# Performance work log

Measured on AMD Instinct MI355X. Metric: run time of the kernel, lower is better.

Reference implementation:

```python
import jax, jax.numpy as jnp
import numpy as np
import math

B, T, E, H = 4, 4096, 1024, 16
D = E // H  # head dim
EPS_DENOM = 1e-6
LN_EPS = 1e-5


def setup_inputs() -> dict:
    key = jax.random.key(0)
    ks = jax.random.split(key, 8)
    s = 0.02
    return {
        "x": jax.random.normal(ks[0], (B, T, E), jnp.float32),
        "ln1_w": jnp.ones((E,), jnp.float32),
        "ln1_b": jnp.zeros((E,), jnp.float32),
        "wq": jax.random.normal(ks[1], (E, E), jnp.float32) * s,
        "bq": jnp.zeros((E,), jnp.float32),
        "wk": jax.random.normal(ks[2], (E, E), jnp.float32) * s,
        "bk": jnp.zeros((E,), jnp.float32),
        "wv": jax.random.normal(ks[3], (E, E), jnp.float32) * s,
        "bv": jnp.zeros((E,), jnp.float32),
        "wo": jax.random.normal(ks[4], (E, E), jnp.float32) * s,
        "bo": jnp.zeros((E,), jnp.float32),
        "ln2_w": jnp.ones((E,), jnp.float32),
        "ln2_b": jnp.zeros((E,), jnp.float32),
        "w_fc": jax.random.normal(ks[5], (E, 4 * E), jnp.float32) * s,
        "b_fc": jnp.zeros((4 * E,), jnp.float32),
        "w_proj": jax.random.normal(ks[6], (4 * E, E), jnp.float32) * s,
        "b_proj": jnp.zeros((E,), jnp.float32),
    }


def _layernorm(x, w, b):
    mu = jnp.mean(x, axis=-1, keepdims=True)
    var = jnp.mean(jnp.square(x - mu), axis=-1, keepdims=True)
    return (x - mu) * jax.lax.rsqrt(var + LN_EPS) * w + b


def _cosformer_attn(x, wq, bq, wk, bk, wv, bv, wo, bo):
    # ReLU feature map on q, k projections
    q = jax.nn.relu(x @ wq + bq)  # [B,T,E]
    k = jax.nn.relu(x @ wk + bk)
    v = x @ wv + bv
    # split heads -> [B,H,T,D]
    q = q.reshape(B, T, H, D).transpose(0, 2, 1, 3)
    k = k.reshape(B, T, H, D).transpose(0, 2, 1, 3)
    v = v.reshape(B, T, H, D).transpose(0, 2, 1, 3)
    # cosine reweighting: idx_i = pi/2 * (i+1)/M, M = T (self-attention)
    idx = (math.pi / 2.0) * jnp.arange(1, T + 1, dtype=x.dtype) / T  # [T]
    s = jnp.sin(idx)[None, None, :, None]
    c = jnp.cos(idx)[None, None, :, None]
    q_ = jnp.concatenate([q * s, q * c], axis=-1)  # [B,H,T,2D]
    k_ = jnp.concatenate([k * s, k * c], axis=-1)  # [B,H,T,2D]
    # non-causal linear attention: O = Q' (K'^T V) / (Q' K'^T 1)
    kv = jnp.einsum("bhtd,bhte->bhde", k_, v)       # [B,H,2D,D]
    z = 1.0 / jnp.maximum(jnp.einsum("bhtd,bhd->bht", q_, k_.sum(axis=2)), EPS_DENOM)
    out = jnp.einsum("bhtd,bhde,bht->bhte", q_, kv, z)  # [B,H,T,D]
    out = out.transpose(0, 2, 1, 3).reshape(B, T, E)
    return out @ wo + bo


def reference(x, ln1_w, ln1_b, wq, bq, wk, bk, wv, bv, wo, bo,
              ln2_w, ln2_b, w_fc, b_fc, w_proj, b_proj):
    h = _layernorm(x, ln1_w, ln1_b)
    x = x + _cosformer_attn(h, wq, bq, wk, bk, wv, bv, wo, bo)
    h = _layernorm(x, ln2_w, ln2_b)
    h = jax.nn.gelu(h @ w_fc + b_fc, approximate=False) @ w_proj + b_proj
    return x + h
```

## Files before the change

kernel.cpp:

```cpp
#include <hip/hip_runtime.h>

#define PI_F 3.14159265358979f
#define MT 16384
#define EE 1024
#define FF 4096
#define NCH 8
#define CHT (4096 / NCH)

typedef unsigned short u16;
typedef __attribute__((ext_vector_type(8))) short short8;
typedef __attribute__((ext_vector_type(4))) float f32x4;

__device__ __forceinline__ float bf2f(u16 u) {
  unsigned int v = ((unsigned int)u) << 16;
  float f;
  __builtin_memcpy(&f, &v, 4);
  return f;
}
__device__ __forceinline__ u16 f2bf(float f) {
  unsigned int x;
  __builtin_memcpy(&x, &f, 4);
  unsigned int r = x + 0x7fffu + ((x >> 16) & 1u);
  return (u16)(r >> 16);
}
__device__ __forceinline__ float ldin(const void* p, long i, int f32) {
  return f32 ? ((const float*)p)[i] : bf2f(((const u16*)p)[i]);
}
__device__ __forceinline__ void async16(const u16* g, u16* l) {
  __builtin_amdgcn_global_load_lds(
      (const __attribute__((address_space(1))) unsigned int*)g,
      (__attribute__((address_space(3))) unsigned int*)l, 16, 0, 0);
}

__global__ __launch_bounds__(256) void detect_dtype(const u16* __restrict__ x,
                                                    int* __restrict__ flag) {
  const int tid = threadIdx.x;
  int cnt = 0;
  for (int i = tid; i < 2048; i += 256) {
    const int e = (x[i] >> 7) & 0xFF;
    if (e == 0 || e >= 0x90) cnt++;
  }
#pragma unroll
  for (int o = 32; o > 0; o >>= 1) cnt += __shfl_xor(cnt, o);
  __shared__ int s[4];
  if ((tid & 63) == 0) s[tid >> 6] = cnt;
  __syncthreads();
  if (tid == 0) flag[0] = (s[0] + s[1] + s[2] + s[3] > 200) ? 1 : 0;
}

__global__ __launch_bounds__(256) void transpose_in(
    const void* __restrict__ src, const int* __restrict__ flag,
    u16* __restrict__ dst, int R, int C) {
  __shared__ float tile[64][65];
  const int f = *flag;
  const int tx = threadIdx.x & 63, ty = threadIdx.x >> 6;
  const long c0 = (long)blockIdx.x * 64, r0 = (long)blockIdx.y * 64;
#pragma unroll
  for (int i = 0; i < 16; i++) {
    const int r = ty + i * 4;
    tile[r][tx] = ldin(src, (r0 + r) * (long)C + c0 + tx, f);
  }
  __syncthreads();
#pragma unroll
  for (int i = 0; i < 16; i++) {
    const int cc = ty + i * 4;
    dst[(c0 + cc) * (long)R + r0 + tx] = f2bf(tile[tx][cc]);
  }
}

__global__ __launch_bounds__(256) void concat3(
    const void* __restrict__ a, const void* __restrict__ b,
    const void* __restrict__ c, const int* __restrict__ flag,
    float* __restrict__ out) {
  const int i = blockIdx.x * 256 + threadIdx.x;
  const int fl = *flag;
  if (i < 1024) out[i] = ldin(a, i, fl);
  else if (i < 2048) out[i] = ldin(b, i - 1024, fl);
  else if (i < 3072) out[i] = ldin(c, i - 2048, fl);
}

__global__ __launch_bounds__(256) void ln_kernel(
    const void* __restrict__ xin, int xmode, const int* __restrict__ flag,
    const void* __restrict__ w, const void* __restrict__ b,
    u16* __restrict__ out) {
  const long row = blockIdx.x;
  const int tid = threadIdx.x;
  const int fl = *flag;
  const int xf = (xmode == 2) ? fl : xmode;
  float v[4];
  if (xf) {
    const float4 q = ((const float4*)((const float*)xin + row * EE))[tid];
    v[0] = q.x; v[1] = q.y; v[2] = q.z; v[3] = q.w;
  } else {
    const ushort4 u = ((const ushort4*)((const u16*)xin + row * EE))[tid];
    v[0] = bf2f(u.x); v[1] = bf2f(u.y); v[2] = bf2f(u.z); v[3] = bf2f(u.w);
  }
  float sum = v[0] + v[1] + v[2] + v[3];
  float sq = v[0] * v[0] + v[1] * v[1] + v[2] * v[2] + v[3] * v[3];
#pragma unroll
  for (int o = 32; o > 0; o >>= 1) {
    sum += __shfl_xor(sum, o);
    sq += __shfl_xor(sq, o);
  }
  __shared__ float s1[4], s2[4];
  const int wave = tid >> 6, lane = tid & 63;
  if (lane == 0) { s1[wave] = sum; s2[wave] = sq; }
  __syncthreads();
  sum = s1[0] + s1[1] + s1[2] + s1[3];
  sq = s2[0] + s2[1] + s2[2] + s2[3];
  const float mu = sum * (1.f / EE);
  const float var = sq * (1.f / EE) - mu * mu;
  const float rs = rsqrtf(var + 1e-5f);
  ushort4 o4;
  float r0 = (v[0] - mu) * rs * ldin(w, tid * 4 + 0, fl) + ldin(b, tid * 4 + 0, fl);
  float r1 = (v[1] - mu) * rs * ldin(w, tid * 4 + 1, fl) + ldin(b, tid * 4 + 1, fl);
  float r2 = (v[2] - mu) * rs * ldin(w, tid * 4 + 2, fl) + ldin(b, tid * 4 + 2, fl);
  float r3 = (v[3] - mu) * rs * ldin(w, tid * 4 + 3, fl) + ldin(b, tid * 4 + 3, fl);
  o4.x = f2bf(r0); o4.y = f2bf(r1); o4.z = f2bf(r2); o4.w = f2bf(r3);
  ((ushort4*)(out + row * EE))[tid] = o4;
}

__global__ __launch_bounds__(512, 2) void gemm256(
    const u16* __restrict__ A, const u16* __restrict__ Bt,
    const void* __restrict__ bias, int biasF32,
    const void* __restrict__ res, int resMode,
    void* __restrict__ Cout, void* __restrict__ Cv, int outMode, long coff,
    const int* __restrict__ flag, int M, int N, int K, int act) {
  __shared__ u16 As[3][2][4096];
  __shared__ u16 Bs[3][2][4096];
  const int tid = threadIdx.x;
  const int lane = tid & 63;
  const int wave = tid >> 6;
  const int wr = wave >> 2;
  const int wc = wave & 3;
  const int quad = lane >> 4;
  const int l16 = lane & 15;
  const int bid0 = blockIdx.x + gridDim.x * blockIdx.y;
  const int width = 4 * gridDim.y;
  const int group = bid0 / width;
  const int rem = bid0 - group * width;
  const int bx = group * 4 + (rem & 3);
  const int by = rem >> 2;
  const long bm = (long)bx * 256;
  const long bn = (long)by * 256;

  f32x4 acc[8][4];
#pragma unroll
  for (int i = 0; i < 8; i++)
#pragma unroll
    for (int j = 0; j < 4; j++)
#pragma unroll
      for (int r = 0; r < 4; r++) acc[i][j][r] = 0.f;

  const int sr = tid >> 2;
  const int su = tid & 3;
  const u16* Ap = A + (bm + sr) * (long)K + su * 8;
  const u16* Bp = Bt + (bn + sr) * (long)K + su * 8;
  const long half128 = 128 * (long)K;

  auto stgA = [&](int d, int h, long kt) {
    async16(Ap + h * half128 + kt, &As[d][h][0] + wave * 512);
  };
  auto stgB = [&](int d, int h, long kt) {
    async16(Bp + h * half128 + kt, &Bs[d][h][0] + wave * 512);
  };

  const int nt = K >> 5;
  stgA(0, 0, 0); stgA(0, 1, 0); stgB(0, 0, 0); stgB(0, 1, 0);
  stgA(1, 0, 32); stgA(1, 1, 32); stgB(1, 0, 32); stgB(1, 1, 32);
  asm volatile("s_waitcnt vmcnt(4)" ::: "memory");
  __builtin_amdgcn_s_barrier();

  int d = 0;
  for (int t = 0; t < nt; ++t) {
    const int sd = (t + 2) % 3;
    const long skt = ((t + 2 < nt) ? (long)(t + 2) : (long)(nt - 1)) * 32;
    const u16* Ah = &As[d][wr][0];
    short8 af[4], bfr[4];
#pragma unroll
    for (int i = 0; i < 4; i++)
      af[i] = *(const short8*)&Ah[(i * 16 + l16) * 32 + quad * 8];
#pragma unroll
    for (int ni = 0; ni < 4; ni++) {
      const int cl = wc * 64 + ni * 16 + l16;
      bfr[ni] = *(const short8*)&Bs[d][cl >> 7][(cl & 127) * 32 + quad * 8];
    }
    stgA(sd, 0, skt);
    stgA(sd, 1, skt);
    asm volatile("s_waitcnt vmcnt(4)" ::: "memory");
    __builtin_amdgcn_s_barrier();
    __builtin_amdgcn_s_setprio(1);
#pragma unroll
    for (int mi = 0; mi < 4; mi++)
#pragma unroll
      for (int ni = 0; ni < 4; ni++)
        acc[mi][ni] = __builtin_amdgcn_mfma_f32_16x16x32_bf16(
            af[mi], bfr[ni], acc[mi][ni], 0, 0, 0);
    __builtin_amdgcn_s_setprio(0);
    __builtin_amdgcn_s_barrier();
#pragma unroll
    for (int i = 0; i < 4; i++)
      af[i] = *(const short8*)&Ah[(64 + i * 16 + l16) * 32 + quad * 8];
    stgB(sd, 0, skt);
    stgB(sd, 1, skt);
    asm volatile("s_waitcnt vmcnt(4)" ::: "memory");
    __builtin_amdgcn_s_barrier();
    __builtin_amdgcn_s_setprio(1);
#pragma unroll
    for (int mi = 0; mi < 4; mi++)
#pragma unroll
      for (int ni = 0; ni < 4; ni++)
        acc[4 + mi][ni] = __builtin_amdgcn_mfma_f32_16x16x32_bf16(
            af[mi], bfr[ni], acc[4 + mi][ni], 0, 0, 0);
    __builtin_amdgcn_s_setprio(0);
    __builtin_amdgcn_s_barrier();
    d = (d == 2) ? 0 : d + 1;
  }
  __syncthreads();

  const int fl = *flag;
  const long Nl = N;
  float bv4[4];
  long gcA[4];
#pragma unroll
  for (int ni = 0; ni < 4; ni++) {
    gcA[ni] = bn + wc * 64 + ni * 16 + l16;
    bv4[ni] = biasF32 ? ((const float*)bias)[gcA[ni]] : ldin(bias, gcA[ni], fl);
  }
#pragma unroll
  for (int mi = 0; mi < 8; mi++)
#pragma unroll
    for (int ni = 0; ni < 4; ni++)
#pragma unroll
      for (int r = 0; r < 4; r++) {
        float v = acc[mi][ni][r] + bv4[ni];
        if (act == 1 || (act == 3 && gcA[ni] < 2048)) v = fmaxf(v, 0.f);
        else if (act == 2) v = 0.5f * v * (1.f + erff(v * 0.70710678118654752f));
        acc[mi][ni][r] = v;
      }
  float* sf = (float*)&As[0][0][0] + wave * 1088;
  const int er = lane >> 2;
  const int ec = (lane & 3) * 16;
#pragma unroll
  for (int mi = 0; mi < 8; mi++) {
#pragma unroll
    for (int ni = 0; ni < 4; ni++)
#pragma unroll
      for (int r = 0; r < 4; r++)
        sf[(quad * 4 + r) * 68 + ni * 16 + l16] = acc[mi][ni][r];
    f32x4 w0 = *(const f32x4*)&sf[er * 68 + ec + 0];
    f32x4 w1 = *(const f32x4*)&sf[er * 68 + ec + 4];
    f32x4 w2 = *(const f32x4*)&sf[er * 68 + ec + 8];
    f32x4 w3 = *(const f32x4*)&sf[er * 68 + ec + 12];
    const long gr = bm + wr * 128 + mi * 16 + er;
    const long gc0 = bn + wc * 64 + ec;
    const long ib = gr * Nl + gc0;
    if (resMode == 1 || (resMode == 2 && fl)) {
      const f32x4* rp = (const f32x4*)((const float*)res + ib);
      f32x4 r0 = rp[0], r1 = rp[1], r2 = rp[2], r3 = rp[3];
#pragma unroll
      for (int j = 0; j < 4; j++) {
        w0[j] += r0[j]; w1[j] += r1[j]; w2[j] += r2[j]; w3[j] += r3[j];
      }
    } else if (resMode == 2) {
      const short8* rp = (const short8*)((const u16*)res + ib);
      short8 ra = rp[0], rb = rp[1];
#pragma unroll
      for (int j = 0; j < 4; j++) {
        w0[j] += bf2f((u16)ra[j]);
        w1[j] += bf2f((u16)ra[j + 4]);
        w2[j] += bf2f((u16)rb[j]);
        w3[j] += bf2f((u16)rb[j + 4]);
      }
    }
    if (outMode == 1 || (outMode == 2 && fl)) {
      f32x4* op = (f32x4*)((float*)Cout + coff + ib);
      op[0] = w0; op[1] = w1; op[2] = w2; op[3] = w3;
    } else {
      u16 tmp[16];
#pragma unroll
      for (int j = 0; j < 4; j++) {
        tmp[j] = f2bf(w0[j]);
        tmp[j + 4] = f2bf(w1[j]);
        tmp[j + 8] = f2bf(w2[j]);
        tmp[j + 12] = f2bf(w3[j]);
      }
      u16* op;
      if (outMode == 3) {
        const int plane = (int)(gc0 >> 10);
        u16* dst = (plane == 2) ? (u16*)Cv
                                : ((u16*)Cout + plane * ((long)M << 10));
        op = dst + (gr << 10) + (gc0 & 1023);
      } else {
        op = (u16*)Cout + coff + ib;
      }
      *(short8*)op = *(short8*)&tmp[0];
      *(short8*)(op + 8) = *(short8*)&tmp[8];
    }
  }
}

__global__ __launch_bounds__(256, 3) void gemm_bf16(
    const u16* __restrict__ A, const u16* __restrict__ Bt,
    const void* __restrict__ bias, int biasF32,
    const void* __restrict__ res, int resMode,
    void* __restrict__ Cout, void* __restrict__ Cv, int outMode, long coff,
    const int* __restrict__ flag, int M, int N, int K, int act) {
  __shared__ u16 As[3][4096];
  __shared__ u16 Bs[3][4096];
  const int tid = threadIdx.x;
  const int lane = tid & 63;
  const int wave = tid >> 6;
  const int quad = lane >> 4;
  const int l16 = lane & 15;
  const int wm = (wave >> 1) * 64;
  const int wn = (wave & 1) * 64;
  const int bid0 = blockIdx.x + gridDim.x * blockIdx.y;
  const int gy = gridDim.y;
  const int width = 8 * gy;
  const int group = bid0 / width;
  const int rem = bid0 - group * width;
  const int bx = group * 8 + (rem & 7);
  const int by = rem >> 3;
  const long bm = (long)bx * 128;
  const long bn = (long)by * 128;

  f32x4 acc[4][4];
#pragma unroll
  for (int i = 0; i < 4; i++)
#pragma unroll
    for (int j = 0; j < 4; j++)
#pragma unroll
      for (int r = 0; r < 4; r++) acc[i][j][r] = 0.f;

  const int trow = tid >> 2;
  const int tswz = (tid & 3) ^ (trow & 3);
  const u16* Ap = A + (bm + trow) * (long)K + tswz * 8;
  const u16* Bp = Bt + (bn + trow) * (long)K + tswz * 8;
  const long rowK64 = 64 * (long)K;

  auto stage = [&](int buf, long kt) {
    u16* Ad = &As[buf][wave * 512];
    u16* Bd = &Bs[buf][wave * 512];
    async16(Ap + kt, Ad);
    async16(Ap + rowK64 + kt, Ad + 2048);
    async16(Bp + kt, Bd);
    async16(Bp + rowK64 + kt, Bd + 2048);
  };
  const int rswz = (quad ^ (l16 & 3)) * 8;
  auto compute = [&](int buf) {
    short8 af[4], bfr[4];
#pragma unroll
    for (int i = 0; i < 4; i++)
      af[i] = *(const short8*)&As[buf][(wm + i * 16 + l16) * 32 + rswz];
#pragma unroll
    for (int i = 0; i < 4; i++)
      bfr[i] = *(const short8*)&Bs[buf][(wn + i * 16 + l16) * 32 + rswz];
    __builtin_amdgcn_s_setprio(1);
#pragma unroll
    for (int mi = 0; mi < 4; mi++)
#pragma unroll
      for (int ni = 0; ni < 4; ni++)
        acc[mi][ni] = __builtin_amdgcn_mfma_f32_16x16x32_bf16(
            af[mi], bfr[ni], acc[mi][ni], 0, 0, 0);
    __builtin_amdgcn_s_setprio(0);
  };

  const int nt = K >> 5;
  stage(0, 0);
  stage(1, 32);
  asm volatile("s_waitcnt vmcnt(4)" ::: "memory");
  __builtin_amdgcn_s_barrier();
  int cb = 0, sb = 2;
  for (int t = 0; t < nt; ++t) {
    const long ts = (t + 2 < nt) ? (long)(t + 2) * 32 : (long)(nt - 1) * 32;
    stage(sb, ts);
    compute(cb);
    asm volatile("s_waitcnt vmcnt(4)" ::: "memory");
    __builtin_amdgcn_s_barrier();
    cb = (cb == 2) ? 0 : cb + 1;
    sb = (sb == 2) ? 0 : sb + 1;
  }
  __syncthreads();

  const int fl = *flag;
  const long Nl = N;
  float bv4[4];
  long gcA[4];
#pragma unroll
  for (int ni = 0; ni < 4; ni++) {
    gcA[ni] = bn + wn + ni * 16 + l16;
    bv4[ni] = biasF32 ? ((const float*)bias)[gcA[ni]] : ldin(bias, gcA[ni], fl);
  }
#pragma unroll
  for (int mi = 0; mi < 4; mi++)
#pragma unroll
    for (int ni = 0; ni < 4; ni++)
#pragma unroll
      for (int r = 0; r < 4; r++) {
        float v = acc[mi][ni][r] + bv4[ni];
        if (act == 1 || (act == 3 && gcA[ni] < 2048)) v = fmaxf(v, 0.f);
        else if (act == 2) v = 0.5f * v * (1.f + erff(v * 0.70710678118654752f));
        acc[mi][ni][r] = v;
      }
  float* sf = (float*)&As[0][0] + wave * 1088;
  const int er = lane >> 2;
  const int ec = (lane & 3) * 16;
#pragma unroll
  for (int mi = 0; mi < 4; mi++) {
#pragma unroll
    for (int ni = 0; ni < 4; ni++)
#pragma unroll
      for (int r = 0; r < 4; r++)
        sf[(quad * 4 + r) * 68 + ni * 16 + l16] = acc[mi][ni][r];
    f32x4 w0 = *(const f32x4*)&sf[er * 68 + ec + 0];
    f32x4 w1 = *(const f32x4*)&sf[er * 68 + ec + 4];
    f32x4 w2 = *(const f32x4*)&sf[er * 68 + ec + 8];
    f32x4 w3 = *(const f32x4*)&sf[er * 68 + ec + 12];
    const long gr = bm + wm + mi * 16 + er;
    const long gc0 = bn + wn + ec;
    const long ib = gr * Nl + gc0;
    if (resMode == 1 || (resMode == 2 && fl)) {
      const f32x4* rp = (const f32x4*)((const float*)res + ib);
      f32x4 r0 = rp[0], r1 = rp[1], r2 = rp[2], r3 = rp[3];
#pragma unroll
      for (int j = 0; j < 4; j++) {
        w0[j] += r0[j]; w1[j] += r1[j]; w2[j] += r2[j]; w3[j] += r3[j];
      }
    } else if (resMode == 2) {
      const short8* rp = (const short8*)((const u16*)res + ib);
      short8 ra = rp[0], rb = rp[1];
#pragma unroll
      for (int j = 0; j < 4; j++) {
        w0[j] += bf2f((u16)ra[j]);
        w1[j] += bf2f((u16)ra[j + 4]);
        w2[j] += bf2f((u16)rb[j]);
        w3[j] += bf2f((u16)rb[j + 4]);
      }
    }
    if (outMode == 1 || (outMode == 2 && fl)) {
      f32x4* op = (f32x4*)((float*)Cout + coff + ib);
      op[0] = w0; op[1] = w1; op[2] = w2; op[3] = w3;
    } else {
      u16 tmp[16];
#pragma unroll
      for (int j = 0; j < 4; j++) {
        tmp[j] = f2bf(w0[j]);
        tmp[j + 4] = f2bf(w1[j]);
        tmp[j + 8] = f2bf(w2[j]);
        tmp[j + 12] = f2bf(w3[j]);
      }
      u16* op;
      if (outMode == 3) {
        const int plane = (int)(bn >> 10);
        u16* dst = (plane == 2) ? (u16*)Cv
                                : ((u16*)Cout + plane * ((long)M << 10));
        op = dst + (gr << 10) + (gc0 & 1023);
      } else {
        op = (u16*)Cout + coff + ib;
      }
      *(short8*)op = *(short8*)&tmp[0];
      *(short8*)(op + 8) = *(short8*)&tmp[8];
    }
  }
}

__global__ __launch_bounds__(256) void kv_partial(
    const u16* __restrict__ k, const u16* __restrict__ v,
    float* __restrict__ kvpart, float* __restrict__ kspart) {
  const int bh = blockIdx.x;
  const int ch = blockIdx.y;
  const int b = bh >> 4, h = bh & 15;
  const int tid = threadIdx.x;
  __shared__ float kl[8][64], vl[8][64];
  const int dkq = tid >> 4;
  const int dvq = tid & 15;
  float accS[4][4] = {}, accC[4][4] = {};
  float ksS[4] = {}, ksC[4] = {};
  const int tt = tid >> 5;
  const int cc = (tid & 31) * 2;
  const long base = ((long)b * 4096 + ch * CHT) * EE + h * 64;
  for (int tb = 0; tb < CHT; tb += 8) {
    const long roff = base + (long)(tb + tt) * EE + cc;
    const unsigned int ku = *(const unsigned int*)(k + roff);
    const unsigned int vu = *(const unsigned int*)(v + roff);
    __syncthreads();
    kl[tt][cc] = bf2f((u16)ku);
    kl[tt][cc + 1] = bf2f((u16)(ku >> 16));
    vl[tt][cc] = bf2f((u16)vu);
    vl[tt][cc + 1] = bf2f((u16)(vu >> 16));
    __syncthreads();
#pragma unroll
    for (int j = 0; j < 8; j++) {
      const int t = ch * CHT + tb + j;
      float s, c;
      __sincosf((float)(t + 1) * (PI_F * 0.5f / 4096.f), &s, &c);
      float kk[4], vv[4];
#pragma unroll
      for (int i = 0; i < 4; i++) {
        kk[i] = kl[j][dkq * 4 + i];
        vv[i] = vl[j][dvq * 4 + i];
      }
#pragma unroll
      for (int i = 0; i < 4; i++) {
        const float ks_ = kk[i] * s, kc_ = kk[i] * c;
        ksS[i] += ks_;
        ksC[i] += kc_;
#pragma unroll
        for (int jj = 0; jj < 4; jj++) {
          accS[i][jj] += ks_ * vv[jj];
          accC[i][jj] += kc_ * vv[jj];
        }
      }
    }
  }
  float* outS = kvpart + (((long)ch * 64 + bh) * 2 + 0) * 4096;
  float* outC = outS + 4096;
#pragma unroll
  for (int i = 0; i < 4; i++)
#pragma unroll
    for (int jj = 0; jj < 4; jj++) {
      outS[(dkq * 4 + i) * 64 + dvq * 4 + jj] = accS[i][jj];
      outC[(dkq * 4 + i) * 64 + dvq * 4 + jj] = accC[i][jj];
    }
  if (dvq == 0) {
    float* oS = kspart + ((long)ch * 64 + bh) * 2 * 64;
#pragma unroll
    for (int i = 0; i < 4; i++) {
      oS[dkq * 4 + i] = ksS[i];
      oS[64 + dkq * 4 + i] = ksC[i];
    }
  }
}

__global__ __launch_bounds__(256) void kv_reduce(
    const float* __restrict__ kvpart, const float* __restrict__ kspart,
    float* __restrict__ kvcomb, float* __restrict__ kscomb) {
  const long KVTOT = 64L * 2 * 4096;
  const long KSTOT = 64L * 2 * 64;
  const long idx = (long)blockIdx.x * 256 + threadIdx.x;
  if (idx < KVTOT) {
    float s = 0.f;
#pragma unroll
    for (int chn = 0; chn < NCH; chn++) s += kvpart[chn * KVTOT + idx];
    kvcomb[idx] = s;
  } else {
    const long i2 = idx - KVTOT;
    if (i2 < KSTOT) {
      float s = 0.f;
#pragma unroll
      for (int chn = 0; chn < NCH; chn++) s += kspart[chn * KSTOT + i2];
      kscomb[i2] = s;
    }
  }
}

__global__ __launch_bounds__(256) void attn_apply(
    const u16* __restrict__ q, const float* __restrict__ kvcomb,
    const float* __restrict__ kscomb, u16* __restrict__ attn) {
  const int bh = blockIdx.x;
  const int b = bh >> 4, h = bh & 15;
  const int t0 = blockIdx.y * 64;
  const int tid = threadIdx.x;
  __shared__ float kvl[2][64][64];
  __shared__ float ksl[2][64];
  __shared__ float ql[64][66];

  const float4* kvsrc = (const float4*)(kvcomb + (long)bh * 8192);
  float4* kvdst = (float4*)&kvl[0][0][0];
#pragma unroll
  for (int i = 0; i < 8; i++) kvdst[tid + 256 * i] = kvsrc[tid + 256 * i];
  if (tid < 32) ((float4*)&ksl[0][0])[tid] = ((const float4*)(kscomb + (long)bh * 128))[tid];
  {
    const int r = tid >> 2;
    const int c = (tid & 3) * 16;
    const u16* qp = q + ((long)b * 4096 + t0 + r) * EE + h * 64 + c;
    const uint4 u0 = *(const uint4*)qp;
    const uint4 u1 = *(const uint4*)(qp + 8);
    unsigned int uu[8] = {u0.x, u0.y, u0.z, u0.w, u1.x, u1.y, u1.z, u1.w};
#pragma unroll
    for (int i = 0; i < 8; i++) {
      ql[r][c + 2 * i] = bf2f((u16)uu[i]);
      ql[r][c + 2 * i + 1] = bf2f((u16)(uu[i] >> 16));
    }
  }
  __syncthreads();

  const int tg = tid >> 4;
  const int dvq = tid & 15;
  const int dv0 = dvq * 4;

  float o1[4][4] = {}, o2[4][4] = {}, zs[4] = {}, zc[4] = {};
  for (int dk = 0; dk < 64; dk++) {
    const float ks0 = ksl[0][dk], ks1 = ksl[1][dk];
    float kv0[4], kv1[4];
#pragma unroll
    for (int j = 0; j < 4; j++) {
      kv0[j] = kvl[0][dk][dv0 + j];
      kv1[j] = kvl[1][dk][dv0 + j];
    }
#pragma unroll
    for (int it = 0; it < 4; it++) {
      const float qv = ql[tg + it * 16][dk];
      zs[it] += qv * ks0;
      zc[it] += qv * ks1;
#pragma unroll
      for (int j = 0; j < 4; j++) {
        o1[it][j] += qv * kv0[j];
        o2[it][j] += qv * kv1[j];
      }
    }
  }
#pragma unroll
  for (int it = 0; it < 4; it++) {
    const int t = t0 + tg + it * 16;
    float s, c;
    __sincosf((float)(t + 1) * (PI_F * 0.5f / 4096.f), &s, &c);
    const float z = s * zs[it] + c * zc[it];
    const float zinv = 1.f / fmaxf(z, 1e-6f);
    ushort4 o4;
    o4.x = f2bf((s * o1[it][0] + c * o2[it][0]) * zinv);
    o4.y = f2bf((s * o1[it][1] + c * o2[it][1]) * zinv);
    o4.z = f2bf((s * o1[it][2] + c * o2[it][2]) * zinv);
    o4.w = f2bf((s * o1[it][3] + c * o2[it][3]) * zinv);
    *(ushort4*)(attn + ((long)b * 4096 + t) * EE + h * 64 + dv0) = o4;
  }
}

extern "C" void kernel_launch(void* const* d_in, const int* in_sizes, int n_in,
                              void* d_out, int out_size, void* d_ws, size_t ws_size,
                              hipStream_t stream) {
  const void* x = d_in[0];
  const void* ln1w = d_in[1];
  const void* ln1b = d_in[2];
  const void* wq = d_in[3];
  const void* bq = d_in[4];
  const void* wk = d_in[5];
  const void* bk = d_in[6];
  const void* wv = d_in[7];
  const void* bv = d_in[8];
  const void* wo = d_in[9];
  const void* bo = d_in[10];
  const void* ln2w = d_in[11];
  const void* ln2b = d_in[12];
  const void* wfc = d_in[13];
  const void* bfc = d_in[14];
  const void* wproj = d_in[15];
  const void* bproj = d_in[16];

  char* ws = (char*)d_ws;
  size_t off = 0;
  auto alloc = [&](size_t bytes) -> char* {
    char* p = ws + off;
    off += (bytes + 255) & ~((size_t)255);
    return p;
  };
  int* flag = (int*)alloc(256);
  u16* wqkvT = (u16*)alloc((size_t)3 * EE * EE * 2);
  u16* woT = (u16*)alloc((size_t)EE * EE * 2);
  u16* wfcT = (u16*)alloc((size_t)EE * FF * 2);
  u16* wprojT = (u16*)alloc((size_t)FF * EE * 2);
  float* qkvBias = (float*)alloc(3072 * 4);
  u16* h = (u16*)alloc((size_t)MT * EE * 2);
  float* x2 = (float*)alloc((size_t)MT * EE * 4);
  u16* qk2 = (u16*)alloc((size_t)2 * MT * EE * 2);
  float* kvpart = (float*)alloc((size_t)NCH * 64 * 2 * 64 * 64 * 4);
  float* kspart = (float*)alloc((size_t)NCH * 64 * 2 * 64 * 4);
  float* kvcomb = (float*)alloc((size_t)64 * 2 * 64 * 64 * 4);
  float* kscomb = (float*)alloc((size_t)64 * 2 * 64 * 4);
  const long PL = (long)MT * EE;
  u16* qb = qk2;
  u16* kb = qk2 + PL;
  u16* vb = (u16*)x2;
  u16* attnb = kb;
  u16* g = qk2;
  (void)ws_size; (void)in_sizes; (void)n_in; (void)out_size;

  detect_dtype<<<1, 256, 0, stream>>>((const u16*)x, flag);

  transpose_in<<<dim3(16, 16), 256, 0, stream>>>(wq, flag, wqkvT, EE, EE);
  transpose_in<<<dim3(16, 16), 256, 0, stream>>>(wk, flag, wqkvT + (size_t)EE * EE, EE, EE);
  transpose_in<<<dim3(16, 16), 256, 0, stream>>>(wv, flag, wqkvT + (size_t)2 * EE * EE, EE, EE);
  transpose_in<<<dim3(16, 16), 256, 0, stream>>>(wo, flag, woT, EE, EE);
  transpose_in<<<dim3(64, 16), 256, 0, stream>>>(wfc, flag, wfcT, EE, FF);
  transpose_in<<<dim3(16, 64), 256, 0, stream>>>(wproj, flag, wprojT, FF, EE);
  concat3<<<12, 256, 0, stream>>>(bq, bk, bv, flag, qkvBias);

  ln_kernel<<<MT, 256, 0, stream>>>(x, 2, flag, ln1w, ln1b, h);

  gemm256<<<dim3(64, 12), 512, 0, stream>>>(h, wqkvT, qkvBias, 1, nullptr, 0,
                                            qk2, vb, 3, 0, flag, MT, 3072, EE, 3);

  kv_partial<<<dim3(64, NCH), 256, 0, stream>>>(kb, vb, kvpart, kspart);
  kv_reduce<<<2080, 256, 0, stream>>>(kvpart, kspart, kvcomb, kscomb);
  attn_apply<<<dim3(64, 64), 256, 0, stream>>>(qb, kvcomb, kscomb, attnb);

  gemm256<<<dim3(64, 4), 512, 0, stream>>>(attnb, woT, bo, 0, x, 2, x2, nullptr,
                                           1, 0, flag, MT, EE, EE, 0);
  ln_kernel<<<MT, 256, 0, stream>>>(x2, 1, flag, ln2w, ln2b, h);

  for (int c = 0; c < 2; c++) {
    const long ro = (long)c * 8192 * EE;
    gemm256<<<dim3(32, 16), 512, 0, stream>>>(h + ro, wfcT, bfc, 0, nullptr, 0,
                                              g, nullptr, 0, 0, flag, 8192, FF, EE, 2);
    gemm_bf16<<<dim3(64, 8), 256, 0, stream>>>(g, wprojT, bproj, 0, x2 + ro, 1,
                                               d_out, nullptr, 2, ro, flag, 8192, EE, FF, 0);
  }
}
```

Measured before the change: 1.148 ms.

## Restructure GEMM main loop to BK=64 double buffering with XOR-swizzled LDS

Changes the 256x256 GEMM mainloop from a triple-buffered K=32 step to a double-buffered K=64 step. Shared memory is laid out with an XOR swizzle on 16-byte chunks to avoid bank conflicts. Each wave now computes a split N tile (two 32-column halves taken from the two B halves) over four sub-phases that interleave async loads with MFMA. The epilogue column mapping is updated to match. The aim is fewer barriers per unit of K and less LDS conflict stalling, at the cost of a larger shared-memory footprint and a shallower prefetch depth.

```diff
diff --git a/kernel.cpp b/kernel.cpp
--- a/kernel.cpp
+++ b/kernel.cpp
@@ -126,8 +126,7 @@
     const void* __restrict__ res, int resMode,
     void* __restrict__ Cout, void* __restrict__ Cv, int outMode, long coff,
     const int* __restrict__ flag, int M, int N, int K, int act) {
-  __shared__ u16 As[3][2][4096];
-  __shared__ u16 Bs[3][2][4096];
+  __shared__ u16 L[2][4][8192];
   const int tid = threadIdx.x;
   const int lane = tid & 63;
   const int wave = tid >> 6;
@@ -152,69 +151,113 @@
 #pragma unroll
       for (int r = 0; r < 4; r++) acc[i][j][r] = 0.f;
 
-  const int sr = tid >> 2;
-  const int su = tid & 3;
-  const u16* Ap = A + (bm + sr) * (long)K + su * 8;
-  const u16* Bp = Bt + (bn + sr) * (long)K + su * 8;
-  const long half128 = 128 * (long)K;
-
-  auto stgA = [&](int d, int h, long kt) {
-    async16(Ap + h * half128 + kt, &As[d][h][0] + wave * 512);
+  const u16* Ap = A + (bm + (lane >> 3)) * (long)K + ((lane & 7) ^ (lane >> 3)) * 8;
+  const u16* Bp = Bt + (bn + (lane >> 3)) * (long)K + ((lane & 7) ^ (lane >> 3)) * 8;
+
+  auto stgA = [&](int dd, int h, long kt) {
+#pragma unroll
+    for (int j = 0; j < 2; j++)
+      async16(Ap + ((long)h * 128 + (j * 8 + wave) * 8) * (long)K + kt,
+              &L[dd][h][(j * 8 + wave) * 512]);
   };
-  auto stgB = [&](int d, int h, long kt) {
-    async16(Bp + h * half128 + kt, &Bs[d][h][0] + wave * 512);
+  auto stgB = [&](int dd, int h, long kt) {
+#pragma unroll
+    for (int j = 0; j < 2; j++)
+      async16(Bp + ((long)h * 128 + (j * 8 + wave) * 8) * (long)K + kt,
+              &L[dd][2 + h][(j * 8 + wave) * 512]);
   };
 
-  const int nt = K >> 5;
+  const int nt = K >> 6;
   stgA(0, 0, 0); stgA(0, 1, 0); stgB(0, 0, 0); stgB(0, 1, 0);
-  stgA(1, 0, 32); stgA(1, 1, 32); stgB(1, 0, 32); stgB(1, 1, 32);
-  asm volatile("s_waitcnt vmcnt(4)" ::: "memory");
-  __builtin_amdgcn_s_barrier();
-
-  int d = 0;
+
   for (int t = 0; t < nt; ++t) {
-    const int sd = (t + 2) % 3;
-    const long skt = ((t + 2 < nt) ? (long)(t + 2) : (long)(nt - 1)) * 32;
-    const u16* Ah = &As[d][wr][0];
-    short8 af[4], bfr[4];
-#pragma unroll
-    for (int i = 0; i < 4; i++)
-      af[i] = *(const short8*)&Ah[(i * 16 + l16) * 32 + quad * 8];
-#pragma unroll
-    for (int ni = 0; ni < 4; ni++) {
-      const int cl = wc * 64 + ni * 16 + l16;
-      bfr[ni] = *(const short8*)&Bs[d][cl >> 7][(cl & 127) * 32 + quad * 8];
+    const int d = t & 1, sd = d ^ 1;
+    const long skt = (long)((t + 1 < nt) ? t + 1 : nt - 1) * 64;
+    const u16* Ah = &L[d][wr][0];
+    const u16* B0h = &L[d][2][0];
+    const u16* B1h = &L[d][3][0];
+    short8 a8[8], bf0[4], bf1[4];
+    asm volatile("s_waitcnt vmcnt(2)" ::: "memory");
+    __builtin_amdgcn_s_barrier();
+#pragma unroll
+    for (int ks = 0; ks < 2; ks++) {
+#pragma unroll
+      for (int mi = 0; mi < 4; mi++) {
+        const int R = mi * 16 + l16;
+        a8[ks * 4 + mi] =
+            *(const short8*)&Ah[R * 64 + ((ks * 4 + quad) ^ (R & 7)) * 8];
+      }
+#pragma unroll
+      for (int ni = 0; ni < 2; ni++) {
+        const int R = wc * 32 + ni * 16 + l16;
+        bf0[ks * 2 + ni] =
+            *(const short8*)&B0h[R * 64 + ((ks * 4 + quad) ^ (R & 7)) * 8];
+      }
     }
     stgA(sd, 0, skt);
+    __builtin_amdgcn_s_setprio(1);
+#pragma unroll
+    for (int mi = 0; mi < 4; mi++)
+#pragma unroll
+      for (int ni = 0; ni < 2; ni++)
+#pragma unroll
+        for (int ks = 0; ks < 2; ks++)
+          acc[mi][ni] = __builtin_amdgcn_mfma_f32_16x16x32_bf16(
+              a8[ks * 4 + mi], bf0[ks * 2 + ni], acc[mi][ni], 0, 0, 0);
+    __builtin_amdgcn_s_setprio(0);
+    asm volatile("s_waitcnt vmcnt(2)" ::: "memory");
+    __builtin_amdgcn_s_barrier();
+#pragma unroll
+    for (int ks = 0; ks < 2; ks++)
+#pragma unroll
+      for (int ni = 0; ni < 2; ni++) {
+        const int R = wc * 32 + ni * 16 + l16;
+        bf1[ks * 2 + ni] =
+            *(const short8*)&B1h[R * 64 + ((ks * 4 + quad) ^ (R & 7)) * 8];
+      }
     stgA(sd, 1, skt);
-    asm volatile("s_waitcnt vmcnt(4)" ::: "memory");
-    __builtin_amdgcn_s_barrier();
     __builtin_amdgcn_s_setprio(1);
 #pragma unroll
     for (int mi = 0; mi < 4; mi++)
 #pragma unroll
-      for (int ni = 0; ni < 4; ni++)
-        acc[mi][ni] = __builtin_amdgcn_mfma_f32_16x16x32_bf16(
-            af[mi], bfr[ni], acc[mi][ni], 0, 0, 0);
+      for (int ni = 0; ni < 2; ni++)
+#pragma unroll
+        for (int ks = 0; ks < 2; ks++)
+          acc[mi][2 + ni] = __builtin_amdgcn_mfma_f32_16x16x32_bf16(
+              a8[ks * 4 + mi], bf1[ks * 2 + ni], acc[mi][2 + ni], 0, 0, 0);
     __builtin_amdgcn_s_setprio(0);
     __builtin_amdgcn_s_barrier();
 #pragma unroll
-    for (int i = 0; i < 4; i++)
-      af[i] = *(const short8*)&Ah[(64 + i * 16 + l16) * 32 + quad * 8];
+    for (int ks = 0; ks < 2; ks++)
+#pragma unroll
+      for (int mi = 0; mi < 4; mi++) {
+        const int R = 64 + mi * 16 + l16;
+        a8[ks * 4 + mi] =
+            *(const short8*)&Ah[R * 64 + ((ks * 4 + quad) ^ (R & 7)) * 8];
+      }
     stgB(sd, 0, skt);
-    stgB(sd, 1, skt);
-    asm volatile("s_waitcnt vmcnt(4)" ::: "memory");
-    __builtin_amdgcn_s_barrier();
     __builtin_amdgcn_s_setprio(1);
 #pragma unroll
     for (int mi = 0; mi < 4; mi++)
 #pragma unroll
-      for (int ni = 0; ni < 4; ni++)
-        acc[4 + mi][ni] = __builtin_amdgcn_mfma_f32_16x16x32_bf16(
-            af[mi], bfr[ni], acc[4 + mi][ni], 0, 0, 0);
+      for (int ni = 0; ni < 2; ni++)
+#pragma unroll
+        for (int ks = 0; ks < 2; ks++)
+          acc[4 + mi][ni] = __builtin_amdgcn_mfma_f32_16x16x32_bf16(
+              a8[ks * 4 + mi], bf0[ks * 2 + ni], acc[4 + mi][ni], 0, 0, 0);
     __builtin_amdgcn_s_setprio(0);
     __builtin_amdgcn_s_barrier();
-    d = (d == 2) ? 0 : d + 1;
+    stgB(sd, 1, skt);
+    __builtin_amdgcn_s_setprio(1);
+#pragma unroll
+    for (int mi = 0; mi < 4; mi++)
+#pragma unroll
+      for (int ni = 0; ni < 2; ni++)
+#pragma unroll
+        for (int ks = 0; ks < 2; ks++)
+          acc[4 + mi][2 + ni] = __builtin_amdgcn_mfma_f32_16x16x32_bf16(
+              a8[ks * 4 + mi], bf1[ks * 2 + ni], acc[4 + mi][2 + ni], 0, 0, 0);
+    __builtin_amdgcn_s_setprio(0);
   }
   __syncthreads();
 
@@ -223,37 +266,43 @@
   float bv4[4];
   long gcA[4];
 #pragma unroll
-  for (int ni = 0; ni < 4; ni++) {
-    gcA[ni] = bn + wc * 64 + ni * 16 + l16;
-    bv4[ni] = biasF32 ? ((const float*)bias)[gcA[ni]] : ldin(bias, gcA[ni], fl);
-  }
-#pragma unroll
-  for (int mi = 0; mi < 8; mi++)
-#pragma unroll
-    for (int ni = 0; ni < 4; ni++)
+  for (int s = 0; s < 2; s++)
+#pragma unroll
+    for (int ni = 0; ni < 2; ni++) {
+      gcA[s * 2 + ni] = bn + s * 128 + wc * 32 + ni * 16 + l16;
+      bv4[s * 2 + ni] = biasF32 ? ((const float*)bias)[gcA[s * 2 + ni]]
+                                : ldin(bias, gcA[s * 2 + ni], fl);
+    }
+#pragma unroll
+  for (int rg = 0; rg < 8; rg++)
+#pragma unroll
+    for (int j = 0; j < 4; j++)
 #pragma unroll
       for (int r = 0; r < 4; r++) {
-        float v = acc[mi][ni][r] + bv4[ni];
-        if (act == 1 || (act == 3 && gcA[ni] < 2048)) v = fmaxf(v, 0.f);
+        float v = acc[rg][j][r] + bv4[j];
+        if (act == 1 || (act == 3 && gcA[j] < 2048)) v = fmaxf(v, 0.f);
         else if (act == 2) v = 0.5f * v * (1.f + erff(v * 0.70710678118654752f));
-        acc[mi][ni][r] = v;
-      }
-  float* sf = (float*)&As[0][0][0] + wave * 1088;
+        acc[rg][j][r] = v;
+      }
+  float* sf = (float*)&L[0][0][0] + wave * 1088;
   const int er = lane >> 2;
   const int ec = (lane & 3) * 16;
 #pragma unroll
-  for (int mi = 0; mi < 8; mi++) {
-#pragma unroll
-    for (int ni = 0; ni < 4; ni++)
-#pragma unroll
-      for (int r = 0; r < 4; r++)
-        sf[(quad * 4 + r) * 68 + ni * 16 + l16] = acc[mi][ni][r];
+  for (int rg = 0; rg < 8; rg++) {
+#pragma unroll
+    for (int s = 0; s < 2; s++)
+#pragma unroll
+      for (int ni = 0; ni < 2; ni++)
+#pragma unroll
+        for (int r = 0; r < 4; r++)
+          sf[(quad * 4 + r) * 68 + s * 32 + ni * 16 + l16] = acc[rg][s * 2 + ni][r];
     f32x4 w0 = *(const f32x4*)&sf[er * 68 + ec + 0];
     f32x4 w1 = *(const f32x4*)&sf[er * 68 + ec + 4];
     f32x4 w2 = *(const f32x4*)&sf[er * 68 + ec + 8];
     f32x4 w3 = *(const f32x4*)&sf[er * 68 + ec + 12];
-    const long gr = bm + wr * 128 + mi * 16 + er;
-    const long gc0 = bn + wc * 64 + ec;
+    const long gr = bm + wr * 128 + rg * 16 + er;
+    const int es = ec >> 5;
+    const long gc0 = bn + es * 128 + wc * 32 + (ec & 31);
     const long ib = gr * Nl + gc0;
     if (resMode == 1 || (resMode == 2 && fl)) {
       const f32x4* rp = (const f32x4*)((const float*)res + ib);
```

Measured after the change: 1.094 ms. 1.05x faster.
